# Performance work log

Hardware: AMD Instinct MI355X
Metric: run time of the kernel (lower is better)

## Reference

```python
import jax, jax.numpy as jnp
import numpy as np

B, T, D = 8, 16, 4096        # batch, query seq len, model size
M = 4096                      # KV cache length
HQ, HK, DK = 32, 8, 128       # q heads, kv heads, head dim
MULT = 0.08838834764831845    # attn_output_multiplier = 1/sqrt(128)
MAX_ATTN = 30.0


def rotate_half(x):
    x1, x2 = jnp.split(x, 2, axis=-1)
    return jnp.concatenate((-x2, x1), axis=-1)


def rope(x, step):
    # x: [B, S, H, DK], step: [B] int
    exponents = jnp.arange(0, DK, 2, dtype=jnp.float32)
    inv_freq = 1.0 / (10000.0 ** (exponents / DK))                  # [DK/2]
    t = jnp.arange(x.shape[1], dtype=jnp.float32)[None, :] + step.astype(jnp.float32)[:, None]  # [B,S]
    phase = jnp.einsum('bi,j->bij', t, inv_freq)                    # [B,S,DK/2]
    phase = jnp.tile(phase, (1, 1, 2))[:, :, None, :]               # [B,S,1,DK]
    return (x * jnp.cos(phase) + rotate_half(x) * jnp.sin(phase)).astype(x.dtype)


def setup_inputs() -> dict:
    key = jax.random.key(0)
    ks = jax.random.split(key, 16)
    inp = {
        'query': jax.random.normal(ks[0], (B, T, D), jnp.float32),
        'key':   jax.random.normal(ks[1], (B, T, D), jnp.float32),
        'value': jax.random.normal(ks[2], (B, T, D), jnp.float32),
        'mask':  jnp.ones((B, 1, T, M), jnp.bool_),
        'mem_k': jax.random.normal(ks[3], (B, M, HK, DK), jnp.float32),
        'mem_v': jax.random.normal(ks[4], (B, M, HK, DK), jnp.float32),
        'step':  jax.random.randint(ks[5], (B,), 0, M - T, jnp.int32),
    }
    # int8 quantized weights + fp32 per-element scales (as in Linear module)
    def qw(kw, ksc, shape):
        w = jax.random.randint(kw, shape, -127, 128, jnp.int32).astype(jnp.int8)
        s = jax.random.uniform(ksc, shape, jnp.float32, 0.005, 0.02)
        return w, s
    inp['wq'], inp['sq'] = qw(ks[6], ks[7], (D, HQ * DK))
    inp['wk'], inp['sk'] = qw(ks[8], ks[9], (D, HK * DK))
    inp['wv'], inp['sv'] = qw(ks[10], ks[11], (D, HK * DK))
    inp['wo'], inp['so'] = qw(ks[12], ks[13], (HQ * DK, D))
    return inp


def reference(query, key, value, mask, mem_k, mem_v, step, wq, sq, wk, sk, wv, sv, wo, so):
    b, t = query.shape[:2]
    # quantized projections (dequant then matmul, as original)
    q = (query @ (wq * sq)).reshape(b, t, HQ, DK)
    k = (key   @ (wk * sk)).reshape(b, t, HK, DK)
    v = (value @ (wv * sv)).reshape(b, t, HK, DK)
    # RoPE with per-batch cache offset
    k = rope(k, step)
    q = rope(q, step)
    # KV cache update
    upd = jax.vmap(lambda m, s, u: jax.lax.dynamic_update_slice_in_dim(m, u, s, axis=0))
    kc = upd(mem_k, step, k)   # [B,M,HK,DK]
    vc = upd(mem_v, step, v)
    new_step = step + t
    memory_mask = (jnp.arange(M) < new_step[:, None])[:, None, None, :]  # [B,1,1,M]
    full_mask = memory_mask * mask                                       # [B,1,T,M] bool
    # grouped-query attention
    g = HQ // HK
    qh = q.reshape(b, t, HK, g, DK)
    logits = jnp.einsum('bthHd,bThd->bhHtT', qh, kc).astype(jnp.float32) * MULT
    logits = MAX_ATTN * jnp.tanh(logits / MAX_ATTN)
    logits = jnp.where(full_mask[:, :, None, :, :], logits, -1e30)
    w = jax.nn.softmax(logits, axis=-1).astype(query.dtype)
    attn = jnp.einsum('bhHtT,bThd->bthHd', w, vc).reshape(b, t, HQ * DK)
    out = attn @ (wo * so)
    return out, kc, vc, new_step
```

## Files before the change

### kernel.cpp

```cpp
#include <hip/hip_runtime.h>
#include <stdint.h>

#define BB 8
#define TT 16
#define DD 4096
#define MM 4096
#define HQ_ 32
#define HK_ 8
#define DK_ 128
#define GQ_ (HQ_/HK_)
#define MULT_ 0.08838834764831845f
#define MAX_ATTN_ 30.0f
#define LN10000_ 9.210340371976184f
#define KSPLIT_ 8
#define KC_ 32

__global__ __launch_bounds__(256) void copy_cache(
    const uint4* __restrict__ mk, const uint4* __restrict__ mv,
    uint4* __restrict__ kc, uint4* __restrict__ vc,
    const int* __restrict__ step, float* __restrict__ ns_out, int zero_rows){
  size_t idx = (size_t)blockIdx.x * 256 + threadIdx.x;
  const size_t n16 = (size_t)BB*MM*HK_*DK_/4;
  if (idx < n16){
    const int b   = (int)(idx >> 20);
    const int pos = (int)((idx >> 8) & (MM-1));
    const unsigned du = (unsigned)(pos - step[b]);
    if (zero_rows && du < (unsigned)TT){
      const uint4 z = {0u,0u,0u,0u};
      kc[idx] = z; vc[idx] = z;
    } else {
      kc[idx] = mk[idx]; vc[idx] = mv[idx];
    }
  }
  if (blockIdx.x == 0 && threadIdx.x < BB)
    ns_out[threadIdx.x] = (float)(step[threadIdx.x] + TT);
}

__global__ __launch_bounds__(256) void zero_ws(float4* __restrict__ a, float4* __restrict__ b){
  const int i = blockIdx.x*256 + threadIdx.x;
  const float4 z = {0.f,0.f,0.f,0.f};
  a[i] = z; b[i] = z;
}

template<int MODE>
__global__ __launch_bounds__(256) void proj_tile(
    const float* __restrict__ Xq, const float* __restrict__ Xk, const float* __restrict__ Xv,
    const int* __restrict__ w0, const float* __restrict__ s0,
    const int* __restrict__ w1, const float* __restrict__ s1,
    const int* __restrict__ w2, const float* __restrict__ s2,
    const int* __restrict__ step,
    float* __restrict__ d0, float* __restrict__ d1, float* __restrict__ d2){
  const int L    = blockIdx.x;
  const int tile = L / KSPLIT_;
  const int ks   = L % KSPLIT_;
  const int tid  = threadIdx.x;

  const float* X; const int* W; const float* S; int wcols, col0, kind;
  if (MODE == 1)      { X = Xq; W = w0; S = s0; wcols = DD;       col0 = tile*DK_;      kind = 3; }
  else if (tile < 32) { X = Xq; W = w0; S = s0; wcols = HQ_*DK_;  col0 = tile*DK_;      kind = 0; }
  else if (tile < 40) { X = Xk; W = w1; S = s1; wcols = HK_*DK_;  col0 = (tile-32)*DK_; kind = 1; }
  else                { X = Xv; W = w2; S = s2; wcols = HK_*DK_;  col0 = (tile-40)*DK_; kind = 2; }

  __shared__ float smem[16384];
  float* Xs = smem;
  float* Ws = smem + 2*KC_*128;

  const int ty = tid >> 4, tx = tid & 15;
  float acc[8][8];
  #pragma unroll
  for (int i=0;i<8;++i)
    #pragma unroll
    for (int j=0;j<8;++j) acc[i][j] = 0.f;

  const int kbase = ks * (DD / KSPLIT_);
  const float4* Xf4 = (const float4*)X;

  float4 xr[4]; int4 wr[4]; float4 sr[4];
  auto STAGE = [&](int ch){
    const int kb = kbase + ch*KC_;
    #pragma unroll
    for (int j=0;j<4;++j){
      const int f = j*256 + tid, r = f>>3, fg = f&7;
      xr[j] = Xf4[(size_t)r*(DD/4) + (kb>>2) + fg];
    }
    #pragma unroll
    for (int j=0;j<4;++j){
      const int e = j*1024 + tid*4, k = e>>7, c = e&127;
      const size_t wi = (size_t)(kb + k)*wcols + col0 + c;
      wr[j] = *(const int4*)(W + wi);
      sr[j] = *(const float4*)(S + wi);
    }
  };
  auto WRITE = [&](int buf){
    #pragma unroll
    for (int j=0;j<4;++j){
      const int f = j*256 + tid, r = f>>3, fg = f&7;
      Xs[(buf*KC_ + fg*4+0)*128 + r] = xr[j].x;
      Xs[(buf*KC_ + fg*4+1)*128 + r] = xr[j].y;
      Xs[(buf*KC_ + fg*4+2)*128 + r] = xr[j].z;
      Xs[(buf*KC_ + fg*4+3)*128 + r] = xr[j].w;
    }
    #pragma unroll
    for (int j=0;j<4;++j){
      const int e = j*1024 + tid*4, k = e>>7, c = e&127;
      const float4 wd = { (float)wr[j].x * sr[j].x, (float)wr[j].y * sr[j].y,
                          (float)wr[j].z * sr[j].z, (float)wr[j].w * sr[j].w };
      *(float4*)&Ws[(buf*KC_ + k)*128 + c] = wd;
    }
  };
  auto COMPUTE = [&](int buf){
    #pragma unroll 8
    for (int kk=0;kk<KC_;++kk){
      const float4 xa = *(const float4*)&Xs[(buf*KC_ + kk)*128 + ty*8];
      const float4 xb = *(const float4*)&Xs[(buf*KC_ + kk)*128 + ty*8 + 4];
      const float4 wa = *(const float4*)&Ws[(buf*KC_ + kk)*128 + tx*8];
      const float4 wb = *(const float4*)&Ws[(buf*KC_ + kk)*128 + tx*8 + 4];
      const float xv_[8] = {xa.x,xa.y,xa.z,xa.w,xb.x,xb.y,xb.z,xb.w};
      const float wv_[8] = {wa.x,wa.y,wa.z,wa.w,wb.x,wb.y,wb.z,wb.w};
      #pragma unroll
      for (int i=0;i<8;++i)
        #pragma unroll
        for (int j=0;j<8;++j)
          acc[i][j] += xv_[i]*wv_[j];
    }
  };

  STAGE(0); WRITE(0);
  int buf = 0;
  const int NCH = (DD/KSPLIT_)/KC_;
  for (int ch=0; ch<NCH; ++ch){
    __syncthreads();
    if (ch+1 < NCH) STAGE(ch+1);
    COMPUTE(buf);
    if (ch+1 < NCH) WRITE(buf^1);
    buf ^= 1;
  }
  __syncthreads();

  if (kind >= 2){
    #pragma unroll
    for (int i=0;i<8;++i){
      const int row = ty*8 + i;
      float* dst;
      if (kind == 3){
        dst = d0 + (size_t)row*DD + col0 + tx*8;
      } else {
        const int b = row >> 4, t = row & 15;
        const int pos = step[b] + t;
        dst = d2 + (((size_t)b*MM + pos)*HK_ + (tile-40))*DK_ + tx*8;
      }
      #pragma unroll
      for (int j=0;j<8;++j) atomicAdd(dst + j, acc[i][j]);
    }
  } else {
    float* Ct = smem;
    #pragma unroll
    for (int i=0;i<8;++i){
      const float4 v0 = {acc[i][0],acc[i][1],acc[i][2],acc[i][3]};
      const float4 v1 = {acc[i][4],acc[i][5],acc[i][6],acc[i][7]};
      *(float4*)&Ct[(ty*8+i)*128 + tx*8]     = v0;
      *(float4*)&Ct[(ty*8+i)*128 + tx*8 + 4] = v1;
    }
    __syncthreads();
    const int col = tid & 127;
    const int rh  = tid >> 7;
    const float invf = expf(-((float)(2*(col & 63)) * (1.0f/DK_)) * LN10000_);
    for (int r = rh*64; r < rh*64 + 64; ++r){
      const float a = Ct[r*128 + col];
      const float p = Ct[r*128 + (col^64)];
      const int b = r >> 4, t = r & 15;
      const int pos = step[b] + t;
      float sn, cs; sincosf((float)pos * invf, &sn, &cs);
      const float o = (col < 64) ? (a*cs - p*sn) : (a*cs + p*sn);
      if (kind == 0)
        atomicAdd(&d0[((((size_t)b*HQ_ + tile)*32 + (col>>2))*TT + t)*4 + (col&3)], o*MULT_);
      else
        atomicAdd(&d1[(((size_t)b*MM + pos)*HK_ + (tile-32))*DK_ + col], o);
    }
  }
}

__global__ __launch_bounds__(256) void qkv_gemm(
    const float* __restrict__ query, const float* __restrict__ key, const float* __restrict__ value,
    const int* __restrict__ wq, const float* __restrict__ sq,
    const int* __restrict__ wk, const float* __restrict__ sk,
    const int* __restrict__ wv, const float* __restrict__ sv,
    const int* __restrict__ step, float* __restrict__ kc, float* __restrict__ vc,
    float* qdst){
  const int b   = blockIdx.x;
  const int hh  = blockIdx.y;
  const int tid = threadIdx.x;
  const int col = tid & 127;
  const int ch  = tid >> 7;

  const float* X; const int* w; const float* s; int wcols, wc, mode;
  if (hh < HQ_)            { mode = 0; X = query; w = wq; s = sq; wcols = HQ_*DK_; wc = hh*DK_ + col; }
  else if (hh < HQ_+HK_)   { mode = 1; X = key;   w = wk; s = sk; wcols = HK_*DK_; wc = (hh-HQ_)*DK_ + col; }
  else                     { mode = 2; X = value; w = wv; s = sv; wcols = HK_*DK_; wc = (hh-HQ_-HK_)*DK_ + col; }

  float acc[TT];
  #pragma unroll
  for (int t=0;t<TT;++t) acc[t] = 0.f;
  const float4* Xb4 = (const float4*)(X + (size_t)b*TT*DD);
  const int*   wp = w + (size_t)(ch*(DD/2))*wcols + wc;
  const float* sp = s + (size_t)(ch*(DD/2))*wcols + wc;
  const int c4_0 = ch*(DD/8);
  for (int c4 = c4_0; c4 < c4_0 + DD/8; ++c4){
    const float wv0 = (float)wp[0]       * sp[0];
    const float wv1 = (float)wp[wcols]   * sp[wcols];
    const float wv2 = (float)wp[2*wcols] * sp[2*wcols];
    const float wv3 = (float)wp[3*wcols] * sp[3*wcols];
    wp += 4*wcols; sp += 4*wcols;
    #pragma unroll
    for (int t=0;t<TT;++t){
      const float4 x4 = Xb4[t*(DD/4) + c4];
      acc[t] += x4.x*wv0 + x4.y*wv1 + x4.z*wv2 + x4.w*wv3;
    }
  }
  __shared__ float pt[2][TT][DK_];
  #pragma unroll
  for (int t=0;t<TT;++t) pt[ch][t][col] = acc[t];
  __syncthreads();
  const int pos_b = step[b];
  const int t0 = ch*8;
  if (mode == 2){
    const int kh = hh - HQ_ - HK_;
    for (int t = t0; t < t0+8; ++t){
      float v_ = pt[0][t][col] + pt[1][t][col];
      vc[(((size_t)b*MM + (pos_b+t))*HK_ + kh)*DK_ + col] = v_;
    }
  } else {
    const float invf = expf(-((float)(2*(col & 63)) * (1.0f/DK_)) * LN10000_);
    for (int t = t0; t < t0+8; ++t){
      const float a = pt[0][t][col]      + pt[1][t][col];
      const float p = pt[0][t][col^64]   + pt[1][t][col^64];
      float sn, cs; sincosf((float)(pos_b + t) * invf, &sn, &cs);
      float o = (col < 64) ? (a*cs - p*sn) : (a*cs + p*sn);
      if (mode == 0){
        o *= MULT_;
        qdst[((size_t)(b*TT + t)*HQ_ + hh)*DK_ + col] = o;
      } else {
        kc[(((size_t)b*MM + (pos_b+t))*HK_ + (hh-HQ_))*DK_ + col] = o;
      }
    }
  }
}

template<bool QWS>
__global__ __launch_bounds__(512) void attn_flash(
    const float* qsrc,
    const int* __restrict__ step,
    const float* __restrict__ kc, const float* __restrict__ vc,
    float* dst){
  const int L  = blockIdx.x;
  const int kh = L & 7;
  const int g  = (L >> 3) & 3;
  const int b  = L >> 5;
  const int h  = kh*GQ_ + g;
  const int tid = threadIdx.x;

  __shared__ float Pt[512][20];
  __shared__ float obuf[TT][DK_];
  __shared__ float m_st[TT], l_st[TT], r_st[TT], cred[TT];
  __shared__ float qs[QWS ? 4 : TT*DK_];

  if (tid < TT){ m_st[tid] = -1e30f; l_st[tid] = 0.f; }
  if constexpr(!QWS){
    const int t = tid >> 5, d4 = tid & 31;
    ((float4*)qs)[t*32 + d4] =
      ((const float4*)qsrc)[ ((size_t)(b*TT + t)*HQ_ + h)*(DK_/4) + d4 ];
  }
  const int limit = step[b] + TT;
  float4 oacc[TT];
  #pragma unroll
  for (int t=0;t<TT;++t){ oacc[t].x=0.f; oacc[t].y=0.f; oacc[t].z=0.f; oacc[t].w=0.f; }
  __syncthreads();

  const int nch = (limit + 511) >> 9;
  for (int cc = 0; cc < nch; ++cc){
    const int c0 = cc << 9;
    const int m  = c0 + tid;
    float S[TT];
    #pragma unroll
    for (int t=0;t<TT;++t) S[t] = 0.f;
    {
      const float4* Kr = (const float4*)(kc + (((size_t)b*MM + m)*HK_ + kh)*DK_);
      if constexpr(QWS){
        const float4* qp = (const float4*)qsrc + ((size_t)b*HQ_ + h)*(32*TT);
        #pragma unroll 4
        for (int i = 0; i < 32; ++i){
          const float4 k4 = Kr[i];
          #pragma unroll
          for (int t = 0; t < TT; ++t){
            const float4 q4 = qp[i*TT + t];
            S[t] += k4.x*q4.x + k4.y*q4.y + k4.z*q4.z + k4.w*q4.w;
          }
        }
      } else {
        #pragma unroll 4
        for (int i = 0; i < 32; ++i){
          const float4 k4 = Kr[i];
          #pragma unroll
          for (int t = 0; t < TT; ++t){
            const float4 q4 = ((const float4*)(qs + t*DK_))[i];
            S[t] += k4.x*q4.x + k4.y*q4.y + k4.z*q4.z + k4.w*q4.w;
          }
        }
      }
    }
    const bool valid = (m < limit);
    #pragma unroll
    for (int t=0;t<TT;++t){
      const float e = __expf(S[t] * (2.0f/MAX_ATTN_));
      const float th = 1.0f - 2.0f/(e + 1.0f);
      S[t] = valid ? (MAX_ATTN_*th) : -1e30f;
    }
#define PACK_S_TO_PT() { float4* pr = (float4*)(&Pt[tid][0]); float4 a_; \
    a_.x=S[0]; a_.y=S[1]; a_.z=S[2]; a_.w=S[3];   pr[0]=a_; \
    a_.x=S[4]; a_.y=S[5]; a_.z=S[6]; a_.w=S[7];   pr[1]=a_; \
    a_.x=S[8]; a_.y=S[9]; a_.z=S[10]; a_.w=S[11]; pr[2]=a_; \
    a_.x=S[12];a_.y=S[13];a_.z=S[14];a_.w=S[15];  pr[3]=a_; }
    PACK_S_TO_PT();
    __syncthreads();
    {
      const int t = tid >> 5, lane = tid & 31;
      float mx = -1e30f;
      #pragma unroll
      for (int j=0;j<16;++j) mx = fmaxf(mx, Pt[lane + 32*j][t]);
      #pragma unroll
      for (int off=16; off>0; off>>=1) mx = fmaxf(mx, __shfl_xor(mx, off));
      if (lane == 0) cred[t] = mx;
    }
    __syncthreads();
    if (tid < TT){
      const float mo = m_st[tid];
      const float mn = fmaxf(mo, cred[tid]);
      r_st[tid] = __expf(mo - mn);
      m_st[tid] = mn;
      l_st[tid] *= r_st[tid];
    }
    __syncthreads();
    #pragma unroll
    for (int t=0;t<TT;++t) S[t] = __expf(S[t] - m_st[t]);
    PACK_S_TO_PT();
#undef PACK_S_TO_PT
    __syncthreads();
    {
      const int t = tid >> 5, lane = tid & 31;
      float sm = 0.f;
      #pragma unroll
      for (int j=0;j<16;++j) sm += Pt[lane + 32*j][t];
      #pragma unroll
      for (int off=16; off>0; off>>=1) sm += __shfl_xor(sm, off);
      if (lane == 0) l_st[t] += sm;
    }
    {
      const int mg = tid >> 5, lane = tid & 31;
      #pragma unroll
      for (int t=0;t<TT;++t){
        const float r = r_st[t];
        oacc[t].x*=r; oacc[t].y*=r; oacc[t].z*=r; oacc[t].w*=r;
      }
      const float* Vb = vc + ((size_t)b*MM*HK_ + kh)*DK_ + lane*4;
      #pragma unroll 2
      for (int j=0;j<32;++j){
        const int ml = mg + 16*j;
        const float4 v4 = *(const float4*)(Vb + (size_t)(c0 + ml)*(HK_*DK_));
        const float4* pp = (const float4*)(&Pt[ml][0]);
        const float4 p0=pp[0], p1=pp[1], p2=pp[2], p3=pp[3];
#define PV1(t, pv) { oacc[t].x += (pv)*v4.x; oacc[t].y += (pv)*v4.y; oacc[t].z += (pv)*v4.z; oacc[t].w += (pv)*v4.w; }
        PV1(0,p0.x)  PV1(1,p0.y)  PV1(2,p0.z)  PV1(3,p0.w)
        PV1(4,p1.x)  PV1(5,p1.y)  PV1(6,p1.z)  PV1(7,p1.w)
        PV1(8,p2.x)  PV1(9,p2.y)  PV1(10,p2.z) PV1(11,p2.w)
        PV1(12,p3.x) PV1(13,p3.y) PV1(14,p3.z) PV1(15,p3.w)
#undef PV1
      }
    }
    __syncthreads();
  }
  {
    const int mg = tid >> 5, lane = tid & 31;
    for (int s = 0; s < 16; ++s){
      if (mg == s){
        #pragma unroll
        for (int t=0;t<TT;++t){
          float4* op = (float4*)(&obuf[t][lane*4]);
          if (s == 0) *op = oacc[t];
          else { float4 c = *op; c.x+=oacc[t].x; c.y+=oacc[t].y; c.z+=oacc[t].z; c.w+=oacc[t].w; *op = c; }
        }
      }
      __syncthreads();
    }
  }
  {
    const int t = tid >> 5, lane = tid & 31;
    const float inv = 1.0f / l_st[t];
    float4 o = *(const float4*)(&obuf[t][lane*4]);
    o.x*=inv; o.y*=inv; o.z*=inv; o.w*=inv;
    ((float4*)dst)[ ((size_t)(b*TT + t)*HQ_ + h)*(DK_/4) + lane ] = o;
  }
}

__global__ __launch_bounds__(256) void out_proj_safe(
    const int* __restrict__ wo, const float* __restrict__ so, float* __restrict__ out){
  int bt = blockIdx.x, tid = threadIdx.x;
  __shared__ float arow[HQ_*DK_];
  float* rowp = out + (size_t)bt*DD;
  for (int c = tid; c < HQ_*DK_; c += 256) arow[c] = rowp[c];
  __syncthreads();
  for (int j = 0; j < 16; ++j){
    int o = j*256 + tid;
    float acc = 0.f;
    for (int c = 0; c < HQ_*DK_; ++c){
      size_t wi = (size_t)c*DD + o;
      acc += arow[c] * (float)wo[wi] * so[wi];
    }
    rowp[o] = acc;
  }
}

extern "C" void kernel_launch(void* const* d_in, const int* in_sizes, int n_in,
                              void* d_out, int out_size, void* d_ws, size_t ws_size,
                              hipStream_t stream) {
  const float* query = (const float*)d_in[0];
  const float* key   = (const float*)d_in[1];
  const float* value = (const float*)d_in[2];
  const float* mem_k = (const float*)d_in[4];
  const float* mem_v = (const float*)d_in[5];
  const int* step  = (const int*)d_in[6];
  const int* wq = (const int*)d_in[7];    const float* sq = (const float*)d_in[8];
  const int* wk = (const int*)d_in[9];    const float* sk = (const float*)d_in[10];
  const int* wv = (const int*)d_in[11];   const float* sv = (const float*)d_in[12];
  const int* wo = (const int*)d_in[13];   const float* so = (const float*)d_in[14];

  float* out  = (float*)d_out;
  float* outA = out;
  float* kcp  = out + (size_t)BB*TT*DD;
  float* vcp  = kcp + (size_t)BB*MM*HK_*DK_;
  float* ns   = vcp + (size_t)BB*MM*HK_*DK_;

  const size_t qsz = (size_t)BB*TT*HQ_*DK_;
  float* qT      = (float*)d_ws;
  float* attn_ws = qT + qsz;
  const int wsmode = (ws_size >= 2*qsz*sizeof(float)) ? 1 : 0;

  copy_cache<<<32768, 256, 0, stream>>>((const uint4*)mem_k, (const uint4*)mem_v,
                                        (uint4*)kcp, (uint4*)vcp, step, ns, wsmode);
  if (wsmode){
    zero_ws<<<512, 256, 0, stream>>>((float4*)qT, (float4*)outA);
    proj_tile<0><<<48*KSPLIT_, 256, 0, stream>>>(query, key, value,
                                                 wq, sq, wk, sk, wv, sv,
                                                 step, qT, kcp, vcp);
    attn_flash<true><<<256, 512, 0, stream>>>(qT, step, kcp, vcp, attn_ws);
    proj_tile<1><<<32*KSPLIT_, 256, 0, stream>>>(attn_ws, nullptr, nullptr,
                                                 wo, so, nullptr, nullptr, nullptr, nullptr,
                                                 step, outA, nullptr, nullptr);
  } else {
    qkv_gemm<<<dim3(BB, HQ_+2*HK_), 256, 0, stream>>>(query, key, value,
                                                      wq, sq, wk, sk, wv, sv,
                                                      step, kcp, vcp, outA);
    attn_flash<false><<<256, 512, 0, stream>>>(outA, step, kcp, vcp, outA);
    out_proj_safe<<<BB*TT, 256, 0, stream>>>(wo, so, outA);
  }
}
```

Before: 1.183 ms.

## Split attention over KV-length chunks with merge kernel, retune projection tiling

Adds a split-KV attention path: attn_split processes each of 4 KV-length chunks per head in separate blocks, writing partial outputs and max/sum statistics, and attn_merge combines them. This raises the attention grid from 256 to 1024 blocks so more compute units stay busy. It also doubles the projection K-split while halving the chunk size, folds workspace zeroing into the cache-copy kernel to save a launch, and applies RoPE in registers via lane shuffles instead of a shared-memory staging pass. The costs are extra workspace, an additional merge launch, and more atomic contention in the projections.

```diff
diff --git a/kernel.cpp b/kernel.cpp
--- a/kernel.cpp
+++ b/kernel.cpp
@@ -12,15 +12,17 @@
 #define MULT_ 0.08838834764831845f
 #define MAX_ATTN_ 30.0f
 #define LN10000_ 9.210340371976184f
-#define KSPLIT_ 8
-#define KC_ 32
+#define KSPLIT_ 16
+#define KC_ 16
+#define MS_ 4
 
 __global__ __launch_bounds__(256) void copy_cache(
     const uint4* __restrict__ mk, const uint4* __restrict__ mv,
     uint4* __restrict__ kc, uint4* __restrict__ vc,
-    const int* __restrict__ step, float* __restrict__ ns_out, int zero_rows){
+    const int* __restrict__ step, float* __restrict__ ns_out, int zero_rows,
+    float4* __restrict__ qT4, float4* __restrict__ outA4){
+  const size_t n16 = (size_t)BB*MM*HK_*DK_/4;
   size_t idx = (size_t)blockIdx.x * 256 + threadIdx.x;
-  const size_t n16 = (size_t)BB*MM*HK_*DK_/4;
   if (idx < n16){
     const int b   = (int)(idx >> 20);
     const int pos = (int)((idx >> 8) & (MM-1));
@@ -31,15 +33,15 @@
     } else {
       kc[idx] = mk[idx]; vc[idx] = mv[idx];
     }
+  } else if (zero_rows){
+    const size_t i = idx - n16;
+    if (i < (size_t)BB*TT*HQ_*DK_/4){
+      const float4 z = {0.f,0.f,0.f,0.f};
+      qT4[i] = z; outA4[i] = z;
+    }
   }
   if (blockIdx.x == 0 && threadIdx.x < BB)
     ns_out[threadIdx.x] = (float)(step[threadIdx.x] + TT);
-}
-
-__global__ __launch_bounds__(256) void zero_ws(float4* __restrict__ a, float4* __restrict__ b){
-  const int i = blockIdx.x*256 + threadIdx.x;
-  const float4 z = {0.f,0.f,0.f,0.f};
-  a[i] = z; b[i] = z;
 }
 
 template<int MODE>
@@ -61,7 +63,7 @@
   else if (tile < 40) { X = Xk; W = w1; S = s1; wcols = HK_*DK_;  col0 = (tile-32)*DK_; kind = 1; }
   else                { X = Xv; W = w2; S = s2; wcols = HK_*DK_;  col0 = (tile-40)*DK_; kind = 2; }
 
-  __shared__ float smem[16384];
+  __shared__ float smem[2*KC_*128*2];
   float* Xs = smem;
   float* Ws = smem + 2*KC_*128;
 
@@ -75,16 +77,16 @@
   const int kbase = ks * (DD / KSPLIT_);
   const float4* Xf4 = (const float4*)X;
 
-  float4 xr[4]; int4 wr[4]; float4 sr[4];
+  float4 xr[2]; int4 wr[2]; float4 sr[2];
   auto STAGE = [&](int ch){
     const int kb = kbase + ch*KC_;
     #pragma unroll
-    for (int j=0;j<4;++j){
-      const int f = j*256 + tid, r = f>>3, fg = f&7;
+    for (int j=0;j<2;++j){
+      const int f = j*256 + tid, r = f>>2, fg = f&3;
       xr[j] = Xf4[(size_t)r*(DD/4) + (kb>>2) + fg];
     }
     #pragma unroll
-    for (int j=0;j<4;++j){
+    for (int j=0;j<2;++j){
       const int e = j*1024 + tid*4, k = e>>7, c = e&127;
       const size_t wi = (size_t)(kb + k)*wcols + col0 + c;
       wr[j] = *(const int4*)(W + wi);
@@ -93,15 +95,15 @@
   };
   auto WRITE = [&](int buf){
     #pragma unroll
-    for (int j=0;j<4;++j){
-      const int f = j*256 + tid, r = f>>3, fg = f&7;
+    for (int j=0;j<2;++j){
+      const int f = j*256 + tid, r = f>>2, fg = f&3;
       Xs[(buf*KC_ + fg*4+0)*128 + r] = xr[j].x;
       Xs[(buf*KC_ + fg*4+1)*128 + r] = xr[j].y;
       Xs[(buf*KC_ + fg*4+2)*128 + r] = xr[j].z;
       Xs[(buf*KC_ + fg*4+3)*128 + r] = xr[j].w;
     }
     #pragma unroll
-    for (int j=0;j<4;++j){
+    for (int j=0;j<2;++j){
       const int e = j*1024 + tid*4, k = e>>7, c = e&127;
       const float4 wd = { (float)wr[j].x * sr[j].x, (float)wr[j].y * sr[j].y,
                           (float)wr[j].z * sr[j].z, (float)wr[j].w * sr[j].w };
@@ -109,7 +111,7 @@
     }
   };
   auto COMPUTE = [&](int buf){
-    #pragma unroll 8
+    #pragma unroll
     for (int kk=0;kk<KC_;++kk){
       const float4 xa = *(const float4*)&Xs[(buf*KC_ + kk)*128 + ty*8];
       const float4 xb = *(const float4*)&Xs[(buf*KC_ + kk)*128 + ty*8 + 4];
@@ -135,7 +137,6 @@
     if (ch+1 < NCH) WRITE(buf^1);
     buf ^= 1;
   }
-  __syncthreads();
 
   if (kind >= 2){
     #pragma unroll
@@ -153,29 +154,28 @@
       for (int j=0;j<8;++j) atomicAdd(dst + j, acc[i][j]);
     }
   } else {
-    float* Ct = smem;
+    const int txl = tx & 7;
+    float invf[8];
+    #pragma unroll
+    for (int j=0;j<8;++j)
+      invf[j] = expf(-((float)(2*(txl*8 + j)) * (1.0f/DK_)) * LN10000_);
     #pragma unroll
     for (int i=0;i<8;++i){
-      const float4 v0 = {acc[i][0],acc[i][1],acc[i][2],acc[i][3]};
-      const float4 v1 = {acc[i][4],acc[i][5],acc[i][6],acc[i][7]};
-      *(float4*)&Ct[(ty*8+i)*128 + tx*8]     = v0;
-      *(float4*)&Ct[(ty*8+i)*128 + tx*8 + 4] = v1;
-    }
-    __syncthreads();
-    const int col = tid & 127;
-    const int rh  = tid >> 7;
-    const float invf = expf(-((float)(2*(col & 63)) * (1.0f/DK_)) * LN10000_);
-    for (int r = rh*64; r < rh*64 + 64; ++r){
-      const float a = Ct[r*128 + col];
-      const float p = Ct[r*128 + (col^64)];
-      const int b = r >> 4, t = r & 15;
+      const int row = ty*8 + i;
+      const int b = row >> 4, t = row & 15;
       const int pos = step[b] + t;
-      float sn, cs; sincosf((float)pos * invf, &sn, &cs);
-      const float o = (col < 64) ? (a*cs - p*sn) : (a*cs + p*sn);
-      if (kind == 0)
-        atomicAdd(&d0[((((size_t)b*HQ_ + tile)*32 + (col>>2))*TT + t)*4 + (col&3)], o*MULT_);
-      else
-        atomicAdd(&d1[(((size_t)b*MM + pos)*HK_ + (tile-32))*DK_ + col], o);
+      #pragma unroll
+      for (int j=0;j<8;++j){
+        const float a = acc[i][j];
+        const float p = __shfl_xor(a, 8);
+        float sn, cs; sincosf((float)pos * invf[j], &sn, &cs);
+        const float o = (tx < 8) ? (a*cs - p*sn) : (a*cs + p*sn);
+        const int col = tx*8 + j;
+        if (kind == 0)
+          atomicAdd(&d0[((((size_t)b*HQ_ + tile)*32 + (col>>2))*TT + t)*4 + (col&3)], o*MULT_);
+        else
+          atomicAdd(&d1[(((size_t)b*MM + pos)*HK_ + (tile-32))*DK_ + col], o);
+      }
     }
   }
 }
@@ -244,6 +244,189 @@
       }
     }
   }
+}
+
+__global__ __launch_bounds__(512) void attn_split(
+    const float* __restrict__ qT, const int* __restrict__ step,
+    const float* __restrict__ kc, const float* __restrict__ vc,
+    float* __restrict__ part_o, float* __restrict__ part_ml){
+  const int L  = blockIdx.x;
+  const int kh = L & 7;
+  const int rr = L >> 3;
+  const int g  = rr & 3;
+  const int ms = (rr >> 2) & 3;
+  const int b  = rr >> 4;
+  const int h  = kh*GQ_ + g;
+  const int tid = threadIdx.x;
+  const int bh = b*HQ_ + h;
+  const size_t po_base = ((size_t)bh*MS_ + ms)*TT*DK_;
+  const size_t ml_base = (((size_t)bh*MS_ + ms)*TT)*2;
+
+  const int limit = step[b] + TT;
+  const int s0 = ms * (MM/MS_);
+  const int s1 = min(s0 + (MM/MS_), limit);
+
+  if (s0 >= limit){
+    float4* po4 = (float4*)(part_o + po_base);
+    const float4 z = {0.f,0.f,0.f,0.f};
+    #pragma unroll
+    for (int q=0;q<4;++q) po4[tid*4+q] = z;
+    if (tid < TT){ part_ml[ml_base + tid*2] = -1e30f; part_ml[ml_base + tid*2+1] = 0.f; }
+    return;
+  }
+
+  __shared__ float Pt[512][20];
+  __shared__ float obuf[TT][DK_];
+  __shared__ float m_st[TT], l_st[TT], r_st[TT], cred[TT];
+
+  if (tid < TT){ m_st[tid] = -1e30f; l_st[tid] = 0.f; }
+  float4 oacc[TT];
+  #pragma unroll
+  for (int t=0;t<TT;++t){ oacc[t].x=0.f; oacc[t].y=0.f; oacc[t].z=0.f; oacc[t].w=0.f; }
+  __syncthreads();
+
+  const int nch = (s1 - s0 + 511) >> 9;
+  for (int cc = 0; cc < nch; ++cc){
+    const int c0 = s0 + (cc << 9);
+    const int m  = c0 + tid;
+    float S[TT];
+    #pragma unroll
+    for (int t=0;t<TT;++t) S[t] = 0.f;
+    {
+      const float4* Kr = (const float4*)(kc + (((size_t)b*MM + m)*HK_ + kh)*DK_);
+      const float4* qp = (const float4*)qT + ((size_t)b*HQ_ + h)*(32*TT);
+      #pragma unroll 4
+      for (int i = 0; i < 32; ++i){
+        const float4 k4 = Kr[i];
+        #pragma unroll
+        for (int t = 0; t < TT; ++t){
+          const float4 q4 = qp[i*TT + t];
+          S[t] += k4.x*q4.x + k4.y*q4.y + k4.z*q4.z + k4.w*q4.w;
+        }
+      }
+    }
+    const bool valid = (m < s1);
+    #pragma unroll
+    for (int t=0;t<TT;++t){
+      const float e = __expf(S[t] * (2.0f/MAX_ATTN_));
+      const float th = 1.0f - 2.0f/(e + 1.0f);
+      S[t] = valid ? (MAX_ATTN_*th) : -1e30f;
+    }
+#define PACK_S_TO_PT() { float4* pr = (float4*)(&Pt[tid][0]); float4 a_; \
+    a_.x=S[0]; a_.y=S[1]; a_.z=S[2]; a_.w=S[3];   pr[0]=a_; \
+    a_.x=S[4]; a_.y=S[5]; a_.z=S[6]; a_.w=S[7];   pr[1]=a_; \
+    a_.x=S[8]; a_.y=S[9]; a_.z=S[10]; a_.w=S[11]; pr[2]=a_; \
+    a_.x=S[12];a_.y=S[13];a_.z=S[14];a_.w=S[15];  pr[3]=a_; }
+    PACK_S_TO_PT();
+    __syncthreads();
+    {
+      const int t = tid >> 5, lane = tid & 31;
+      float mx = -1e30f;
+      #pragma unroll
+      for (int j=0;j<16;++j) mx = fmaxf(mx, Pt[lane + 32*j][t]);
+      #pragma unroll
+      for (int off=16; off>0; off>>=1) mx = fmaxf(mx, __shfl_xor(mx, off));
+      if (lane == 0) cred[t] = mx;
+    }
+    __syncthreads();
+    if (tid < TT){
+      const float mo = m_st[tid];
+      const float mn = fmaxf(mo, cred[tid]);
+      r_st[tid] = __expf(mo - mn);
+      m_st[tid] = mn;
+      l_st[tid] *= r_st[tid];
+    }
+    __syncthreads();
+    #pragma unroll
+    for (int t=0;t<TT;++t) S[t] = __expf(S[t] - m_st[t]);
+    PACK_S_TO_PT();
+#undef PACK_S_TO_PT
+    __syncthreads();
+    {
+      const int t = tid >> 5, lane = tid & 31;
+      float sm = 0.f;
+      #pragma unroll
+      for (int j=0;j<16;++j) sm += Pt[lane + 32*j][t];
+      #pragma unroll
+      for (int off=16; off>0; off>>=1) sm += __shfl_xor(sm, off);
+      if (lane == 0) l_st[t] += sm;
+    }
+    {
+      const int mg = tid >> 5, lane = tid & 31;
+      #pragma unroll
+      for (int t=0;t<TT;++t){
+        const float r = r_st[t];
+        oacc[t].x*=r; oacc[t].y*=r; oacc[t].z*=r; oacc[t].w*=r;
+      }
+      const float* Vb = vc + ((size_t)b*MM*HK_ + kh)*DK_ + lane*4;
+      #pragma unroll 2
+      for (int j=0;j<32;++j){
+        const int ml = mg + 16*j;
+        const float4 v4 = *(const float4*)(Vb + (size_t)(c0 + ml)*(HK_*DK_));
+        const float4* pp = (const float4*)(&Pt[ml][0]);
+        const float4 p0=pp[0], p1=pp[1], p2=pp[2], p3=pp[3];
+#define PV1(t, pv) { oacc[t].x += (pv)*v4.x; oacc[t].y += (pv)*v4.y; oacc[t].z += (pv)*v4.z; oacc[t].w += (pv)*v4.w; }
+        PV1(0,p0.x)  PV1(1,p0.y)  PV1(2,p0.z)  PV1(3,p0.w)
+        PV1(4,p1.x)  PV1(5,p1.y)  PV1(6,p1.z)  PV1(7,p1.w)
+        PV1(8,p2.x)  PV1(9,p2.y)  PV1(10,p2.z) PV1(11,p2.w)
+        PV1(12,p3.x) PV1(13,p3.y) PV1(14,p3.z) PV1(15,p3.w)
+#undef PV1
+      }
+    }
+    __syncthreads();
+  }
+  {
+    const int mg = tid >> 5, lane = tid & 31;
+    for (int s = 0; s < 16; ++s){
+      if (mg == s){
+        #pragma unroll
+        for (int t=0;t<TT;++t){
+          float4* op = (float4*)(&obuf[t][lane*4]);
+          if (s == 0) *op = oacc[t];
+          else { float4 c = *op; c.x+=oacc[t].x; c.y+=oacc[t].y; c.z+=oacc[t].z; c.w+=oacc[t].w; *op = c; }
+        }
+      }
+      __syncthreads();
+    }
+  }
+  {
+    const int t = tid >> 5, lane = tid & 31;
+    ((float4*)(part_o + po_base))[t*32 + lane] = *(const float4*)(&obuf[t][lane*4]);
+    if (tid < TT){
+      part_ml[ml_base + tid*2]   = m_st[tid];
+      part_ml[ml_base + tid*2+1] = l_st[tid];
+    }
+  }
+}
+
+__global__ __launch_bounds__(512) void attn_merge(
+    const float* __restrict__ part_o, const float* __restrict__ part_ml,
+    float* __restrict__ dst){
+  const int bh = blockIdx.x;
+  const int b = bh >> 5, h = bh & 31;
+  const int tid = threadIdx.x;
+  const int t = tid >> 5, lane = tid & 31;
+  float m[MS_], l[MS_];
+  #pragma unroll
+  for (int ms=0; ms<MS_; ++ms){
+    const size_t mlb = (((size_t)bh*MS_ + ms)*TT + t)*2;
+    m[ms] = part_ml[mlb]; l[ms] = part_ml[mlb+1];
+  }
+  float M = -1e30f;
+  #pragma unroll
+  for (int ms=0; ms<MS_; ++ms) M = fmaxf(M, m[ms]);
+  float Ls = 0.f; float w[MS_];
+  #pragma unroll
+  for (int ms=0; ms<MS_; ++ms){ w[ms] = __expf(m[ms]-M); Ls += l[ms]*w[ms]; }
+  float4 o = {0.f,0.f,0.f,0.f};
+  #pragma unroll
+  for (int ms=0; ms<MS_; ++ms){
+    const float4 po = ((const float4*)(part_o + (((size_t)bh*MS_+ms)*TT + t)*DK_))[lane];
+    o.x += w[ms]*po.x; o.y += w[ms]*po.y; o.z += w[ms]*po.z; o.w += w[ms]*po.w;
+  }
+  const float inv = 1.0f / Ls;
+  o.x*=inv; o.y*=inv; o.z*=inv; o.w*=inv;
+  ((float4*)dst)[ ((size_t)(b*TT + t)*HQ_ + h)*32 + lane ] = o;
 }
 
 template<bool QWS>
@@ -439,20 +622,38 @@
   float* vcp  = kcp + (size_t)BB*MM*HK_*DK_;
   float* ns   = vcp + (size_t)BB*MM*HK_*DK_;
 
-  const size_t qsz = (size_t)BB*TT*HQ_*DK_;
+  const size_t qsz   = (size_t)BB*TT*HQ_*DK_;
+  const size_t posz  = (size_t)BB*HQ_*MS_*TT*DK_;
+  const size_t mlsz  = (size_t)BB*HQ_*MS_*TT*2;
   float* qT      = (float*)d_ws;
-  float* attn_ws = qT + qsz;
-  const int wsmode = (ws_size >= 2*qsz*sizeof(float)) ? 1 : 0;
-
-  copy_cache<<<32768, 256, 0, stream>>>((const uint4*)mem_k, (const uint4*)mem_v,
-                                        (uint4*)kcp, (uint4*)vcp, step, ns, wsmode);
-  if (wsmode){
-    zero_ws<<<512, 256, 0, stream>>>((float4*)qT, (float4*)outA);
+  float* part_o  = qT + qsz;
+  float* part_ml = part_o + posz;
+  float* attn_s  = part_ml + mlsz;
+  float* attn_m  = qT + qsz;
+
+  const size_t need_split = (qsz + posz + mlsz + qsz) * sizeof(float);
+  const int wsmode = (ws_size >= need_split) ? 2
+                   : (ws_size >= 2*qsz*sizeof(float)) ? 1 : 0;
+
+  copy_cache<<<32768 + (wsmode ? 512 : 0), 256, 0, stream>>>(
+      (const uint4*)mem_k, (const uint4*)mem_v, (uint4*)kcp, (uint4*)vcp,
+      step, ns, wsmode ? 1 : 0, (float4*)qT, (float4*)outA);
+
+  if (wsmode == 2){
     proj_tile<0><<<48*KSPLIT_, 256, 0, stream>>>(query, key, value,
                                                  wq, sq, wk, sk, wv, sv,
                                                  step, qT, kcp, vcp);
-    attn_flash<true><<<256, 512, 0, stream>>>(qT, step, kcp, vcp, attn_ws);
-    proj_tile<1><<<32*KSPLIT_, 256, 0, stream>>>(attn_ws, nullptr, nullptr,
+    attn_split<<<BB*MS_*GQ_*HK_, 512, 0, stream>>>(qT, step, kcp, vcp, part_o, part_ml);
+    attn_merge<<<BB*HQ_, 512, 0, stream>>>(part_o, part_ml, attn_s);
+    proj_tile<1><<<32*KSPLIT_, 256, 0, stream>>>(attn_s, nullptr, nullptr,
+                                                 wo, so, nullptr, nullptr, nullptr, nullptr,
+                                                 step, outA, nullptr, nullptr);
+  } else if (wsmode == 1){
+    proj_tile<0><<<48*KSPLIT_, 256, 0, stream>>>(query, key, value,
+                                                 wq, sq, wk, sk, wv, sv,
+                                                 step, qT, kcp, vcp);
+    attn_flash<true><<<256, 512, 0, stream>>>(qT, step, kcp, vcp, attn_m);
+    proj_tile<1><<<32*KSPLIT_, 256, 0, stream>>>(attn_m, nullptr, nullptr,
                                                  wo, so, nullptr, nullptr, nullptr, nullptr,
                                                  step, outA, nullptr, nullptr);
   } else {
```

New measurement: 1.850 ms. +56.4%, slower.
